# Performance work log

Hardware: AMD Instinct MI355X
Metric: run time of the kernel (lower is better)

Reference implementation:

```python
import jax, jax.numpy as jnp
import numpy as np

B, S, H, NH = 2, 2048, 1024, 16
DK = H // NH

def setup_inputs() -> dict:
    key = jax.random.key(0)
    ks = jax.random.split(key, 8)
    scale = 0.02
    return {
        "x": jax.random.normal(ks[0], (B, S, H), jnp.float32),
        "mask": jax.random.randint(ks[1], (B, S, S), 0, 2, jnp.int32),
        "alibi": jax.random.normal(ks[2], (1, NH, S, S), jnp.float32),
        "W_q": jax.random.normal(ks[3], (H, H), jnp.float32) * scale,
        "b_q": jnp.zeros((H,), jnp.float32),
        "W_k": jax.random.normal(ks[4], (H, H), jnp.float32) * scale,
        "b_k": jnp.zeros((H,), jnp.float32),
        "W_v": jax.random.normal(ks[5], (H, H), jnp.float32) * scale,
        "b_v": jnp.zeros((H,), jnp.float32),
        "W_o": jax.random.normal(ks[6], (H, H), jnp.float32) * scale,
        "b_o": jnp.zeros((H,), jnp.float32),
    }

def reference(x, mask, alibi, W_q, b_q, W_k, b_k, W_v, b_v, W_o, b_o):
    b, s, h = x.shape
    def split_heads(t):  # [B,S,H] -> [B,NH,S,DK]
        return t.reshape(b, s, NH, DK).transpose(0, 2, 1, 3)
    q = split_heads(x @ W_q + b_q)
    k = split_heads(x @ W_k + b_k)
    v = split_heads(x @ W_v + b_v)
    scores = jnp.einsum("bhqd,bhkd->bhqk", q, k) / jnp.sqrt(jnp.float32(DK))
    scores = scores + alibi
    scores = jnp.where(mask[:, None, :, :] == 0, jnp.float32(-1e9), scores)
    probs = jax.nn.softmax(scores, axis=-1)  # dropout is identity in eval
    ctx = jnp.einsum("bhqk,bhkd->bhqd", probs, v)
    ctx = ctx.transpose(0, 2, 1, 3).reshape(b, s, h)
    return ctx @ W_o + b_o
```

## Files before the change

### kernel.cpp

```cpp
#include <hip/hip_runtime.h>
#include <hip/hip_bf16.h>


#define S_LEN 2048
#define H_DIM 1024
#define N_HEADS 16

typedef __bf16 bf16x8 __attribute__((ext_vector_type(8)));
typedef __bf16 bf16x4 __attribute__((ext_vector_type(4)));
typedef float f32x4 __attribute__((ext_vector_type(4)));
typedef unsigned long long u64;

using gvoid = __attribute__((address_space(1))) void;
using svoid = __attribute__((address_space(3))) void;

static __device__ __forceinline__ f32x4 mfma16(bf16x8 a, bf16x8 b, f32x4 c) {
  return __builtin_amdgcn_mfma_f32_16x16x32_bf16(a, b, c, 0, 0, 0);
}

template <int NCH, int NW>
static __device__ __forceinline__ void stage64(const __bf16* g, int rstride,
                                               __bf16* lds, int wid, int lane) {
#pragma unroll
  for (int i = 0; i < NCH / NW; ++i) {
    int chunk = i * NW + wid;
    int u = chunk * 64 + lane;
    int r = u >> 3, s = u & 7;
    const __bf16* src = g + (size_t)r * rstride + ((s ^ (r & 7)) << 3);
    __builtin_amdgcn_global_load_lds((const gvoid*)src,
                                     (svoid*)(lds + chunk * 512), 16, 0, 0);
  }
}

static __device__ __forceinline__ bf16x8 read_frag(const __bf16* lds, int r,
                                                   int slot) {
  return *(const bf16x8*)(lds + r * 64 + ((slot ^ (r & 7)) << 3));
}

__global__ __launch_bounds__(256) void k_convert_x(const float* __restrict__ x,
                                                   __bf16* __restrict__ xb) {
  size_t idx = ((size_t)blockIdx.x * 256 + threadIdx.x) * 8;
  float4 a = *(const float4*)(x + idx);
  float4 b = *(const float4*)(x + idx + 4);
  bf16x8 o;
  o[0] = (__bf16)a.x; o[1] = (__bf16)a.y; o[2] = (__bf16)a.z; o[3] = (__bf16)a.w;
  o[4] = (__bf16)b.x; o[5] = (__bf16)b.y; o[6] = (__bf16)b.z; o[7] = (__bf16)b.w;
  *(bf16x8*)(xb + idx) = o;
}

__global__ __launch_bounds__(256) void k_transpose_w(
    const float* __restrict__ w0, const float* __restrict__ w1,
    const float* __restrict__ w2, const float* __restrict__ w3,
    __bf16* __restrict__ wt) {
  __shared__ float t[64][65];
  int z = blockIdx.z;
  const float* W = (z == 0) ? w0 : (z == 1) ? w1 : (z == 2) ? w2 : w3;
  __bf16* O = wt + (size_t)z * H_DIM * H_DIM;
  int k0 = blockIdx.x * 64, n0 = blockIdx.y * 64;
  int tid = threadIdx.x;
  {
    int r = tid >> 4, c4 = tid & 15;
#pragma unroll
    for (int i = 0; i < 4; ++i) {
      float4 v = *(const float4*)(W + (size_t)(k0 + r + i * 16) * H_DIM + n0 + c4 * 4);
      t[r + i * 16][c4 * 4 + 0] = v.x;
      t[r + i * 16][c4 * 4 + 1] = v.y;
      t[r + i * 16][c4 * 4 + 2] = v.z;
      t[r + i * 16][c4 * 4 + 3] = v.w;
    }
  }
  __syncthreads();
  {
    int nn = tid >> 2, js = (tid & 3) * 16;
    bf16x8 o0, o1;
#pragma unroll
    for (int j = 0; j < 8; ++j) {
      o0[j] = (__bf16)t[js + j][nn];
      o1[j] = (__bf16)t[js + 8 + j][nn];
    }
    __bf16* dst = O + (size_t)(n0 + nn) * H_DIM + k0 + js;
    *(bf16x8*)dst = o0;
    *(bf16x8*)(dst + 8) = o1;
  }
}

__global__ __launch_bounds__(256) void k_pack_mask(const int* __restrict__ m,
                                                   u64* __restrict__ out) {
  size_t idx = (size_t)blockIdx.x * 256 + threadIdx.x;
  u64 b = __ballot(m[idx] != 0);
  if ((threadIdx.x & 63) == 0) out[idx >> 6] = b;
}

template <int MODE>
__global__ __launch_bounds__(256) void k_gemm(
    const __bf16* __restrict__ A, const __bf16* __restrict__ B0,
    const __bf16* __restrict__ B1, const __bf16* __restrict__ B2,
    const float* __restrict__ bias0, const float* __restrict__ bias1,
    const float* __restrict__ bias2, __bf16* __restrict__ O0,
    __bf16* __restrict__ O1, __bf16* __restrict__ O2, float* __restrict__ Of) {
  __shared__ alignas(16) __bf16 As[128 * 64];
  __shared__ alignas(16) __bf16 Bs[128 * 64];
  int tid = threadIdx.x, wid = tid >> 6, lane = tid & 63;
  int l15 = lane & 15, lg = lane >> 4;
  int nbase = blockIdx.x * 128, mbase = blockIdx.y * 128;
  const __bf16* Bm;
  const float* bias;
  __bf16* Ob;
  float oscale = 1.0f;
  const int zv = (MODE == 0) ? blockIdx.z : 0;
  if (MODE == 0) {
    Bm = (zv == 0) ? B0 : (zv == 1) ? B1 : B2;
    bias = (zv == 0) ? bias0 : (zv == 1) ? bias1 : bias2;
    Ob = (zv == 0) ? O0 : (zv == 1) ? O1 : O2;
    if (zv == 0) oscale = 0.125f;
  } else {
    Bm = B0; bias = bias0; Ob = O0;
  }
  int wrow = wid >> 1, wcol = wid & 1;
  f32x4 zero = {0.f, 0.f, 0.f, 0.f};
  f32x4 acc[4][4];
#pragma unroll
  for (int i = 0; i < 4; ++i)
#pragma unroll
    for (int j = 0; j < 4; ++j) acc[i][j] = zero;

  for (int kb = 0; kb < H_DIM; kb += 64) {
    __syncthreads();
    const __bf16* Abase;
    int arstride;
    if (MODE == 0) {
      Abase = A + (size_t)mbase * H_DIM + kb;
      arstride = H_DIM;
    } else {
      int b = mbase >> 11, q0 = mbase & 2047, head = kb >> 6;
      Abase = A + ((size_t)(b * N_HEADS + head) * S_LEN + q0) * 64;
      arstride = 64;
    }
    stage64<16, 4>(Abase, arstride, As, wid, lane);
    stage64<16, 4>(Bm + (size_t)nbase * H_DIM + kb, H_DIM, Bs, wid, lane);
    __syncthreads();
#pragma unroll
    for (int t = 0; t < 2; ++t) {
      bf16x8 a[4], bfr[4];
#pragma unroll
      for (int i = 0; i < 4; ++i)
        a[i] = read_frag(As, wrow * 64 + i * 16 + l15, t * 4 + lg);
#pragma unroll
      for (int j = 0; j < 4; ++j)
        bfr[j] = read_frag(Bs, wcol * 64 + j * 16 + l15, t * 4 + lg);
#pragma unroll
      for (int i = 0; i < 4; ++i)
#pragma unroll
        for (int j = 0; j < 4; ++j) acc[i][j] = mfma16(a[i], bfr[j], acc[i][j]);
    }
  }
  float bv[4];
#pragma unroll
  for (int j = 0; j < 4; ++j) bv[j] = bias[nbase + wcol * 64 + j * 16 + l15];
#pragma unroll
  for (int i = 0; i < 4; ++i)
#pragma unroll
    for (int j = 0; j < 4; ++j) {
      if (MODE == 0 && zv == 2) {
        int m0 = mbase + wrow * 64 + i * 16 + lg * 4;
        int col = nbase + wcol * 64 + j * 16 + l15;
        bf16x4 u;
#pragma unroll
        for (int r = 0; r < 4; ++r) u[r] = (__bf16)(acc[i][j][r] + bv[j]);
        size_t off =
            (((size_t)(m0 >> 11) * N_HEADS + (col >> 6)) * 64 + (col & 63)) *
                (size_t)S_LEN +
            (m0 & 2047);
        *(bf16x4*)(Ob + off) = u;
      } else {
#pragma unroll
        for (int r = 0; r < 4; ++r) {
          int m = mbase + wrow * 64 + i * 16 + lg * 4 + r;
          int col = nbase + wcol * 64 + j * 16 + l15;
          float v = (acc[i][j][r] + bv[j]) * oscale;
          if (MODE == 0) {
            size_t off =
                (((size_t)(m >> 11) * N_HEADS + (col >> 6)) * S_LEN +
                 (m & 2047)) *
                    64 +
                (col & 63);
            Ob[off] = (__bf16)v;
          } else {
            Of[(size_t)m * H_DIM + col] = v;
          }
        }
      }
    }
}

__global__ __launch_bounds__(512) void k_attn(
    const __bf16* __restrict__ Q, const __bf16* __restrict__ K,
    const __bf16* __restrict__ VT, const float* __restrict__ alibi,
    const u64* __restrict__ maskb, float* __restrict__ Op,
    float* __restrict__ ml) {
  __shared__ alignas(16) __bf16 Ks[2][64 * 64];
  __shared__ alignas(16) __bf16 Vs[64 * 64];
  __shared__ alignas(16) __bf16 Ps[8][16 * 72];
  int tid = threadIdx.x, wid = tid >> 6, lane = tid & 63;
  int l15 = lane & 15, lg = lane >> 4;
  int bh = blockIdx.x;
  int b = bh & 1, h = bh >> 1;
  int qbase = blockIdx.y * 128;
  const int z = blockIdx.z;
  size_t bho = (size_t)(b * N_HEADS + h);
  const __bf16* Qb = Q + bho * S_LEN * 64;
  const __bf16* Kbz = K + (bho * S_LEN + (size_t)z * 1024) * 64;
  const __bf16* Vbz = VT + bho * 64 * S_LEN + z * 1024;
  const int q = qbase + wid * 16 + l15;
  const int NT = 16;

  bf16x8 qa[2];
  {
    const __bf16* qrow = Qb + (size_t)q * 64;
    qa[0] = *(const bf16x8*)(qrow + lg * 8);
    qa[1] = *(const bf16x8*)(qrow + 32 + lg * 8);
  }
  float mrun = -__builtin_inff(), lrun = 0.f;
  f32x4 cacc[4];
  f32x4 zero = {0.f, 0.f, 0.f, 0.f};
#pragma unroll
  for (int c = 0; c < 4; ++c) cacc[c] = zero;

  const float* arow =
      alibi + ((size_t)h * S_LEN + q) * S_LEN + z * 1024 + lg * 4;
  const u64* mrow =
      maskb + ((size_t)b * S_LEN + q) * (S_LEN / 64) + z * 16;

  stage64<8, 8>(Kbz, 64, Ks[0], wid, lane);
  __builtin_amdgcn_sched_barrier(0);
  f32x4 albP[4];
  u64 mskP;
#pragma unroll
  for (int c = 0; c < 4; ++c) albP[c] = *(const f32x4*)(arow + c * 16);
  mskP = mrow[0];
  __builtin_amdgcn_sched_barrier(0);

  for (int t = 0; t < NT; ++t) {
    const int cur = t & 1;
    asm volatile("s_waitcnt vmcnt(5)" ::: "memory");
    __builtin_amdgcn_sched_barrier(0);
    __builtin_amdgcn_s_barrier();
    __builtin_amdgcn_sched_barrier(0);
    stage64<8, 8>(Vbz + t * 64, S_LEN, Vs, wid, lane);
    __builtin_amdgcn_sched_barrier(0);
    const int tn = (t + 1 < NT) ? t + 1 : t;
    stage64<8, 8>(Kbz + (size_t)tn * 64 * 64, 64, Ks[cur ^ 1], wid, lane);
    __builtin_amdgcn_sched_barrier(0);

    f32x4 sacc[4];
#pragma unroll
    for (int c = 0; c < 4; ++c) sacc[c] = albP[c];
    __builtin_amdgcn_s_setprio(1);
#pragma unroll
    for (int t2 = 0; t2 < 2; ++t2) {
      bf16x8 kf[4];
#pragma unroll
      for (int c = 0; c < 4; ++c)
        kf[c] = read_frag(Ks[cur], c * 16 + l15, t2 * 4 + lg);
#pragma unroll
      for (int c = 0; c < 4; ++c) sacc[c] = mfma16(kf[c], qa[t2], sacc[c]);
    }
    __builtin_amdgcn_s_setprio(0);
    u64 sh = mskP >> (lg * 4);
#pragma unroll
    for (int c = 0; c < 4; ++c)
      albP[c] = *(const f32x4*)(arow + tn * 64 + c * 16);
    mskP = mrow[tn];

    float m16 = -__builtin_inff();
#pragma unroll
    for (int c = 0; c < 4; ++c) {
      unsigned bits = (unsigned)(sh >> (c * 16)) & 0xFu;
#pragma unroll
      for (int r = 0; r < 4; ++r) {
        float v = (bits & (1u << r)) ? sacc[c][r] : -1e9f;
        sacc[c][r] = v;
        m16 = fmaxf(m16, v);
      }
    }
    m16 = fmaxf(m16, __shfl_xor(m16, 16));
    m16 = fmaxf(m16, __shfl_xor(m16, 32));
    const bool norsc = __all(m16 <= mrun);
    float mn = fmaxf(mrun, m16);
    float scl = __expf(mrun - mn);
    mrun = mn;
    float rs = 0.f;
#pragma unroll
    for (int c = 0; c < 4; ++c)
#pragma unroll
      for (int r = 0; r < 4; ++r) {
        float pe = __expf(sacc[c][r] - mn);
        sacc[c][r] = pe;
        rs += pe;
      }
    rs += __shfl_xor(rs, 16);
    rs += __shfl_xor(rs, 32);
    lrun = lrun * scl + rs;
    if (!norsc) {
#pragma unroll
      for (int c = 0; c < 4; ++c) {
        f32x4 v = cacc[c];
        v[0] *= scl; v[1] *= scl; v[2] *= scl; v[3] *= scl;
        cacc[c] = v;
      }
    }
#pragma unroll
    for (int c = 0; c < 4; ++c) {
      bf16x4 u;
#pragma unroll
      for (int r = 0; r < 4; ++r) u[r] = (__bf16)sacc[c][r];
      *(bf16x4*)(&Ps[wid][l15 * 72 + c * 16 + lg * 4]) = u;
    }
    __builtin_amdgcn_sched_barrier(0);
    asm volatile("s_waitcnt vmcnt(6)" ::: "memory");
    __builtin_amdgcn_sched_barrier(0);
    __builtin_amdgcn_s_barrier();
    __builtin_amdgcn_sched_barrier(0);
    __builtin_amdgcn_s_setprio(1);
#pragma unroll
    for (int t2 = 0; t2 < 2; ++t2) {
      bf16x8 pa = *(const bf16x8*)(&Ps[wid][l15 * 72 + t2 * 32 + lg * 8]);
#pragma unroll
      for (int c = 0; c < 4; ++c) {
        bf16x8 vb = read_frag(Vs, c * 16 + l15, t2 * 4 + lg);
        cacc[c] = mfma16(vb, pa, cacc[c]);
      }
    }
    __builtin_amdgcn_s_setprio(0);
  }
  asm volatile("s_waitcnt vmcnt(0)" ::: "memory");
  float* op = Op + (((size_t)z * 32 + bho) * S_LEN + q) * 64;
#pragma unroll
  for (int c = 0; c < 4; ++c) *(f32x4*)(op + c * 16 + lg * 4) = cacc[c];
  if (lg == 0) {
    float2* mlp = (float2*)(ml + (((size_t)z * 32 + bho) * S_LEN + q) * 2);
    *mlp = make_float2(mrun, lrun);
  }
}

__global__ __launch_bounds__(256) void k_combine(const float* __restrict__ Op,
                                                 const float* __restrict__ ml,
                                                 __bf16* __restrict__ ctx) {
  int t = blockIdx.x * 256 + threadIdx.x;
  int dgrp = t & 15, qq = t >> 4;
  float2 m0 = *(const float2*)(ml + (size_t)qq * 2);
  float2 m1 = *(const float2*)(ml + ((size_t)65536 + qq) * 2);
  float m = fmaxf(m0.x, m1.x);
  float e0 = __expf(m0.x - m), e1 = __expf(m1.x - m);
  float inv = 1.f / (m0.y * e0 + m1.y * e1);
  f32x4 a = *(const f32x4*)(Op + (size_t)qq * 64 + dgrp * 4);
  f32x4 c = *(const f32x4*)(Op + (size_t)65536 * 64 + (size_t)qq * 64 + dgrp * 4);
  bf16x4 o;
#pragma unroll
  for (int j = 0; j < 4; ++j) o[j] = (__bf16)((a[j] * e0 + c[j] * e1) * inv);
  *(bf16x4*)(ctx + (size_t)qq * 64 + dgrp * 4) = o;
}

extern "C" void kernel_launch(void* const* d_in, const int* in_sizes, int n_in,
                              void* d_out, int out_size, void* d_ws,
                              size_t ws_size, hipStream_t stream) {
  const float* x = (const float*)d_in[0];
  const int* mask = (const int*)d_in[1];
  const float* alibi = (const float*)d_in[2];
  const float* Wq = (const float*)d_in[3];
  const float* bq = (const float*)d_in[4];
  const float* Wk = (const float*)d_in[5];
  const float* bk = (const float*)d_in[6];
  const float* Wv = (const float*)d_in[7];
  const float* bv = (const float*)d_in[8];
  const float* Wo = (const float*)d_in[9];
  const float* bo = (const float*)d_in[10];
  float* out = (float*)d_out;
  char* ws = (char*)d_ws;

  const size_t MB = 1u << 20;
  __bf16* xb = (__bf16*)(ws);
  __bf16* wt = (__bf16*)(ws + 8 * MB);
  __bf16* Qb = (__bf16*)(ws + 16 * MB);
  __bf16* Kb = (__bf16*)(ws + 24 * MB);
  __bf16* VTb = (__bf16*)(ws + 32 * MB);
  u64* maskb = (u64*)(ws + 40 * MB);
  float* Op = (float*)(ws + 48 * MB);
  float* mlb = (float*)(ws + 112 * MB);
  __bf16* ctxb = xb;
  __bf16* wtq = wt;
  __bf16* wtk = wt + (1u << 20);
  __bf16* wtv = wt + 2 * (1u << 20);
  __bf16* wto = wt + 3 * (1u << 20);

  k_convert_x<<<dim3(2048), 256, 0, stream>>>(x, xb);
  k_transpose_w<<<dim3(16, 16, 4), 256, 0, stream>>>(Wq, Wk, Wv, Wo, wt);
  k_gemm<0><<<dim3(8, 32, 3), 256, 0, stream>>>(xb, wtq, wtk, wtv, bq, bk, bv,
                                                Qb, Kb, VTb, nullptr);
  k_pack_mask<<<dim3((2 * S_LEN * S_LEN) / 256), 256, 0, stream>>>(mask, maskb);
  k_attn<<<dim3(32, 16, 2), 512, 0, stream>>>(Qb, Kb, VTb, alibi, maskb, Op,
                                              mlb);
  k_combine<<<dim3(4096), 256, 0, stream>>>(Op, mlb, ctxb);
  k_gemm<1><<<dim3(8, 32, 1), 256, 0, stream>>>(ctxb, wto, nullptr, nullptr, bo,
                                                nullptr, nullptr, nullptr,
                                                nullptr, nullptr, out);
}
```

Baseline: 240.5 us.

## Merge prep kernels into one launch, store split-K partials in bf16, reorder heads

Result: faster. 226.2 us (median of 2 runs) (-5.9%).

```diff
diff --git a/kernel.cpp b/kernel.cpp
--- a/kernel.cpp
+++ b/kernel.cpp
@@ -37,58 +37,59 @@
   return *(const bf16x8*)(lds + r * 64 + ((slot ^ (r & 7)) << 3));
 }
 
-__global__ __launch_bounds__(256) void k_convert_x(const float* __restrict__ x,
-                                                   __bf16* __restrict__ xb) {
-  size_t idx = ((size_t)blockIdx.x * 256 + threadIdx.x) * 8;
-  float4 a = *(const float4*)(x + idx);
-  float4 b = *(const float4*)(x + idx + 4);
-  bf16x8 o;
-  o[0] = (__bf16)a.x; o[1] = (__bf16)a.y; o[2] = (__bf16)a.z; o[3] = (__bf16)a.w;
-  o[4] = (__bf16)b.x; o[5] = (__bf16)b.y; o[6] = (__bf16)b.z; o[7] = (__bf16)b.w;
-  *(bf16x8*)(xb + idx) = o;
-}
-
-__global__ __launch_bounds__(256) void k_transpose_w(
+__global__ __launch_bounds__(256) void k_prep(
+    const float* __restrict__ x, __bf16* __restrict__ xb,
+    const int* __restrict__ m, u64* __restrict__ mout,
     const float* __restrict__ w0, const float* __restrict__ w1,
     const float* __restrict__ w2, const float* __restrict__ w3,
     __bf16* __restrict__ wt) {
-  __shared__ float t[64][65];
-  int z = blockIdx.z;
-  const float* W = (z == 0) ? w0 : (z == 1) ? w1 : (z == 2) ? w2 : w3;
-  __bf16* O = wt + (size_t)z * H_DIM * H_DIM;
-  int k0 = blockIdx.x * 64, n0 = blockIdx.y * 64;
-  int tid = threadIdx.x;
-  {
-    int r = tid >> 4, c4 = tid & 15;
-#pragma unroll
-    for (int i = 0; i < 4; ++i) {
-      float4 v = *(const float4*)(W + (size_t)(k0 + r + i * 16) * H_DIM + n0 + c4 * 4);
-      t[r + i * 16][c4 * 4 + 0] = v.x;
-      t[r + i * 16][c4 * 4 + 1] = v.y;
-      t[r + i * 16][c4 * 4 + 2] = v.z;
-      t[r + i * 16][c4 * 4 + 3] = v.w;
-    }
-  }
-  __syncthreads();
-  {
-    int nn = tid >> 2, js = (tid & 3) * 16;
-    bf16x8 o0, o1;
-#pragma unroll
-    for (int j = 0; j < 8; ++j) {
-      o0[j] = (__bf16)t[js + j][nn];
-      o1[j] = (__bf16)t[js + 8 + j][nn];
-    }
-    __bf16* dst = O + (size_t)(n0 + nn) * H_DIM + k0 + js;
-    *(bf16x8*)dst = o0;
-    *(bf16x8*)(dst + 8) = o1;
-  }
-}
-
-__global__ __launch_bounds__(256) void k_pack_mask(const int* __restrict__ m,
-                                                   u64* __restrict__ out) {
-  size_t idx = (size_t)blockIdx.x * 256 + threadIdx.x;
-  u64 b = __ballot(m[idx] != 0);
-  if ((threadIdx.x & 63) == 0) out[idx >> 6] = b;
+  int blk = blockIdx.x;
+  if (blk < 2048) {
+    size_t idx = ((size_t)blk * 256 + threadIdx.x) * 8;
+    float4 a = *(const float4*)(x + idx);
+    float4 b = *(const float4*)(x + idx + 4);
+    bf16x8 o;
+    o[0] = (__bf16)a.x; o[1] = (__bf16)a.y; o[2] = (__bf16)a.z; o[3] = (__bf16)a.w;
+    o[4] = (__bf16)b.x; o[5] = (__bf16)b.y; o[6] = (__bf16)b.z; o[7] = (__bf16)b.w;
+    *(bf16x8*)(xb + idx) = o;
+  } else if (blk < 34816) {
+    size_t idx = (size_t)(blk - 2048) * 256 + threadIdx.x;
+    u64 b = __ballot(m[idx] != 0);
+    if ((threadIdx.x & 63) == 0) mout[idx >> 6] = b;
+  } else {
+    __shared__ float t[64][65];
+    int i = blk - 34816;
+    int z = i >> 8;
+    const float* W = (z == 0) ? w0 : (z == 1) ? w1 : (z == 2) ? w2 : w3;
+    __bf16* O = wt + (size_t)z * H_DIM * H_DIM;
+    int k0 = ((i >> 4) & 15) * 64, n0 = (i & 15) * 64;
+    int tid = threadIdx.x;
+    {
+      int r = tid >> 4, c4 = tid & 15;
+#pragma unroll
+      for (int j = 0; j < 4; ++j) {
+        float4 v =
+            *(const float4*)(W + (size_t)(k0 + r + j * 16) * H_DIM + n0 + c4 * 4);
+        t[r + j * 16][c4 * 4 + 0] = v.x;
+        t[r + j * 16][c4 * 4 + 1] = v.y;
+        t[r + j * 16][c4 * 4 + 2] = v.z;
+        t[r + j * 16][c4 * 4 + 3] = v.w;
+      }
+    }
+    __syncthreads();
+    {
+      int nn = tid >> 2, js = (tid & 3) * 16;
+      bf16x8 o0, o1;
+#pragma unroll
+      for (int j = 0; j < 8; ++j) {
+        o0[j] = (__bf16)t[js + j][nn];
+        o1[j] = (__bf16)t[js + 8 + j][nn];
+      }
+      __bf16* dst = O + (size_t)(n0 + nn) * H_DIM + k0 + js;
+      *(bf16x8*)dst = o0;
+      *(bf16x8*)(dst + 8) = o1;
+    }
+  }
 }
 
 template <int MODE>
@@ -196,7 +197,7 @@
 __global__ __launch_bounds__(512) void k_attn(
     const __bf16* __restrict__ Q, const __bf16* __restrict__ K,
     const __bf16* __restrict__ VT, const float* __restrict__ alibi,
-    const u64* __restrict__ maskb, float* __restrict__ Op,
+    const u64* __restrict__ maskb, __bf16* __restrict__ Op,
     float* __restrict__ ml) {
   __shared__ alignas(16) __bf16 Ks[2][64 * 64];
   __shared__ alignas(16) __bf16 Vs[64 * 64];
@@ -204,7 +205,7 @@
   int tid = threadIdx.x, wid = tid >> 6, lane = tid & 63;
   int l15 = lane & 15, lg = lane >> 4;
   int bh = blockIdx.x;
-  int b = bh & 1, h = bh >> 1;
+  int b = bh >> 4, h = bh & 15;
   int qbase = blockIdx.y * 128;
   const int z = blockIdx.z;
   size_t bho = (size_t)(b * N_HEADS + h);
@@ -334,16 +335,21 @@
     __builtin_amdgcn_s_setprio(0);
   }
   asm volatile("s_waitcnt vmcnt(0)" ::: "memory");
-  float* op = Op + (((size_t)z * 32 + bho) * S_LEN + q) * 64;
-#pragma unroll
-  for (int c = 0; c < 4; ++c) *(f32x4*)(op + c * 16 + lg * 4) = cacc[c];
+  __bf16* op = Op + (((size_t)z * 32 + bho) * S_LEN + q) * 64;
+#pragma unroll
+  for (int c = 0; c < 4; ++c) {
+    bf16x4 u;
+#pragma unroll
+    for (int r = 0; r < 4; ++r) u[r] = (__bf16)cacc[c][r];
+    *(bf16x4*)(op + c * 16 + lg * 4) = u;
+  }
   if (lg == 0) {
     float2* mlp = (float2*)(ml + (((size_t)z * 32 + bho) * S_LEN + q) * 2);
     *mlp = make_float2(mrun, lrun);
   }
 }
 
-__global__ __launch_bounds__(256) void k_combine(const float* __restrict__ Op,
+__global__ __launch_bounds__(256) void k_combine(const __bf16* __restrict__ Op,
                                                  const float* __restrict__ ml,
                                                  __bf16* __restrict__ ctx) {
   int t = blockIdx.x * 256 + threadIdx.x;
@@ -353,11 +359,12 @@
   float m = fmaxf(m0.x, m1.x);
   float e0 = __expf(m0.x - m), e1 = __expf(m1.x - m);
   float inv = 1.f / (m0.y * e0 + m1.y * e1);
-  f32x4 a = *(const f32x4*)(Op + (size_t)qq * 64 + dgrp * 4);
-  f32x4 c = *(const f32x4*)(Op + (size_t)65536 * 64 + (size_t)qq * 64 + dgrp * 4);
+  bf16x4 a = *(const bf16x4*)(Op + (size_t)qq * 64 + dgrp * 4);
+  bf16x4 c = *(const bf16x4*)(Op + (size_t)65536 * 64 + (size_t)qq * 64 + dgrp * 4);
   bf16x4 o;
 #pragma unroll
-  for (int j = 0; j < 4; ++j) o[j] = (__bf16)((a[j] * e0 + c[j] * e1) * inv);
+  for (int j = 0; j < 4; ++j)
+    o[j] = (__bf16)(((float)a[j] * e0 + (float)c[j] * e1) * inv);
   *(bf16x4*)(ctx + (size_t)qq * 64 + dgrp * 4) = o;
 }
 
@@ -385,19 +392,18 @@
   __bf16* Kb = (__bf16*)(ws + 24 * MB);
   __bf16* VTb = (__bf16*)(ws + 32 * MB);
   u64* maskb = (u64*)(ws + 40 * MB);
-  float* Op = (float*)(ws + 48 * MB);
-  float* mlb = (float*)(ws + 112 * MB);
+  __bf16* Op = (__bf16*)(ws + 48 * MB);
+  float* mlb = (float*)(ws + 72 * MB);
   __bf16* ctxb = xb;
   __bf16* wtq = wt;
   __bf16* wtk = wt + (1u << 20);
   __bf16* wtv = wt + 2 * (1u << 20);
   __bf16* wto = wt + 3 * (1u << 20);
 
-  k_convert_x<<<dim3(2048), 256, 0, stream>>>(x, xb);
-  k_transpose_w<<<dim3(16, 16, 4), 256, 0, stream>>>(Wq, Wk, Wv, Wo, wt);
+  k_prep<<<dim3(2048 + (2 * S_LEN * S_LEN) / 256 + 1024), 256, 0, stream>>>(
+      x, xb, mask, maskb, Wq, Wk, Wv, Wo, wt);
   k_gemm<0><<<dim3(8, 32, 3), 256, 0, stream>>>(xb, wtq, wtk, wtv, bq, bk, bv,
                                                 Qb, Kb, VTb, nullptr);
-  k_pack_mask<<<dim3((2 * S_LEN * S_LEN) / 256), 256, 0, stream>>>(mask, maskb);
   k_attn<<<dim3(32, 16, 2), 512, 0, stream>>>(Qb, Kb, VTb, alibi, maskb, Op,
                                               mlb);
   k_combine<<<dim3(4096), 256, 0, stream>>>(Op, mlb, ctxb);
```
